# Kernel optimization log

Hardware: AMD Instinct MI355X
Metric: run time of the kernel (lower is better)

## Reference

```python
import jax, jax.numpy as jnp
import numpy as np

N = 4096          # rank / n
OFF_DIAG = 4      # banded half-width
D_IN = 4096       # v: [N, D_IN]
D_OUT = 4096      # u: [D_OUT, N]
BATCH, SEQ = 4, 2048


def _banded_indices(n, off_diag):
    """All (row, col) entries of the 2*off_diag+1 diagonals, like torch.sparse.spdiags."""
    rows, cols = [], []
    for off in range(-off_diag, off_diag + 1):
        if off >= 0:
            i = np.arange(0, n - off)
        else:
            i = np.arange(-off, n)
        rows.append(i)
        cols.append(i + off)
    return np.concatenate(rows).astype(np.int32), np.concatenate(cols).astype(np.int32)


def setup_inputs() -> dict:
    key = jax.random.key(0)
    k_x, k_u, k_v, k_sp, k_s = jax.random.split(key, 5)
    row, col = _banded_indices(N, OFF_DIAG)
    nnz = row.shape[0]  # 36844
    return {
        "x": jax.random.normal(k_x, (BATCH, SEQ, D_IN), dtype=jnp.float32),
        "u": jax.random.normal(k_u, (D_OUT, N), dtype=jnp.float32),
        "v": jax.random.normal(k_v, (N, D_IN), dtype=jnp.float32),
        "s_pre": jax.random.uniform(k_sp, (N,), dtype=jnp.float32),  # singular values (diag)
        # kaiming_normal_ on a [1, nnz] tensor -> std = sqrt(2 / nnz)
        "s": jax.random.normal(k_s, (nnz,), dtype=jnp.float32) * np.float32(np.sqrt(2.0 / nnz)),
        "gate": jnp.zeros((1,), dtype=jnp.float32),
        "row": jnp.asarray(row),
        "col": jnp.asarray(col),
    }


def reference(x, u, v, s_pre, s, gate, row, col):
    n = s_pre.shape[0]
    # del_s = diag(s_pre) + scatter(s * sigmoid(gate)) at banded indices  -> [n, n]
    vals = s * jax.nn.sigmoid(gate)          # [nnz]
    M = jnp.zeros((n, n), dtype=x.dtype).at[row, col].add(vals)
    M = M.at[jnp.arange(n), jnp.arange(n)].add(s_pre)
    # weight = ((del_s @ v).T) @ u.T  -> [D_IN, D_OUT]
    weight = (M @ v).T @ u.T
    return x @ weight
```

## Files before the change

kernel.cpp:

```cpp
#include <hip/hip_runtime.h>
#include <cstdint>

typedef unsigned short u16;
typedef __attribute__((ext_vector_type(8))) __bf16 bf16x8;
typedef __attribute__((ext_vector_type(4))) float f32x4;

#define N_DIM 4096

__device__ __forceinline__ u16 f2bf(float f) {
    union { float f; unsigned u; } c; c.f = f;
    unsigned u = c.u;
    u += 0x7FFFu + ((u >> 16) & 1u);
    return (u16)(u >> 16);
}

__device__ __forceinline__ void gl_lds16(const u16* g, u16* l) {
    __builtin_amdgcn_global_load_lds(
        (const __attribute__((address_space(1))) void*)g,
        (__attribute__((address_space(3))) void*)l, 16, 0, 0);
}

__global__ void band_kernel(const float* __restrict__ s,
                            const float* __restrict__ s_pre,
                            const float* __restrict__ gate,
                            float* __restrict__ bnd) {
    int n = blockIdx.x * blockDim.x + threadIdx.x;
    if (n >= N_DIM) return;
    float sig = 1.0f / (1.0f + __expf(-gate[0]));
    const int base[9] = {0, 4092, 8185, 12279, 16374, 20470, 24565, 28659, 32752};
    #pragma unroll
    for (int o = 0; o < 9; ++o) {
        int off = o - 4;
        int col = n + off;
        float val = 0.0f;
        if (col >= 0 && col < N_DIM) {
            int idx = (off >= 0) ? (base[o] + n) : (base[o] + n + off);
            val = s[idx] * sig;
        }
        if (off == 0) val += s_pre[n];
        bnd[n * 9 + o] = val;
    }
}

__global__ void band_combine_t(const float* __restrict__ v,
                               const float* __restrict__ bnd,
                               u16* __restrict__ P) {
    __shared__ float tile[32][33];
    int n0 = blockIdx.x * 32;
    int d0 = blockIdx.y * 32;
    int tx = threadIdx.x;
    int ty = threadIdx.y;
    #pragma unroll
    for (int i = 0; i < 4; ++i) {
        int nl = ty + 8 * i;
        int n = n0 + nl;
        int d = d0 + tx;
        float acc = 0.0f;
        #pragma unroll
        for (int o = 0; o < 9; ++o) {
            int src = n + o - 4;
            float w = bnd[n * 9 + o];
            float vv = ((unsigned)src < (unsigned)N_DIM) ? v[(size_t)src * N_DIM + d] : 0.0f;
            acc += w * vv;
        }
        tile[nl][tx] = acc;
    }
    __syncthreads();
    #pragma unroll
    for (int i = 0; i < 4; ++i) {
        int dl = ty + 8 * i;
        P[(size_t)(d0 + dl) * N_DIM + (n0 + tx)] = f2bf(tile[tx][dl]);
    }
}

__global__ void cvt_bf16(const float* __restrict__ in, u16* __restrict__ out, int nElem4) {
    int i = blockIdx.x * blockDim.x + threadIdx.x;
    if (i >= nElem4) return;
    float4 f = ((const float4*)in)[i];
    ushort4 o;
    o.x = f2bf(f.x); o.y = f2bf(f.y); o.z = f2bf(f.z); o.w = f2bf(f.w);
    ((ushort4*)out)[i] = o;
}

template <bool OUT_BF16>
__global__ __launch_bounds__(256)
void gemm_tn(const u16* __restrict__ A, const u16* __restrict__ B,
             float* __restrict__ Cf, u16* __restrict__ Cb,
             int M, int N, int K) {
    __shared__ u16 As[128 * 32];
    __shared__ u16 Bs[128 * 32];
    const int tid = threadIdx.x;
    const int lane = tid & 63;
    const int wave = tid >> 6;
    const int wm = wave >> 1;
    const int wn = wave & 1;
    const long m0 = (long)blockIdx.y * 128;
    const long n0 = (long)blockIdx.x * 128;

    const u16* Ab = A + m0 * K;
    const u16* Bb = B + n0 * K;

    f32x4 acc[4][4];
    #pragma unroll
    for (int i = 0; i < 4; ++i)
        #pragma unroll
        for (int j = 0; j < 4; ++j)
            acc[i][j] = (f32x4){0.f, 0.f, 0.f, 0.f};

    const int row = tid >> 2;
    const int kc  = (tid & 3) * 8;

    const int ml = lane & 15;
    const int kq = (lane >> 4) * 8;

    for (int kt = 0; kt < K; kt += 32) {
        __syncthreads();
        gl_lds16(Ab + (long)row * K + kt + kc,        &As[tid * 8]);
        gl_lds16(Ab + (long)(row + 64) * K + kt + kc, &As[2048 + tid * 8]);
        gl_lds16(Bb + (long)row * K + kt + kc,        &Bs[tid * 8]);
        gl_lds16(Bb + (long)(row + 64) * K + kt + kc, &Bs[2048 + tid * 8]);
        __syncthreads();

        bf16x8 af[4], bfr[4];
        #pragma unroll
        for (int i = 0; i < 4; ++i)
            af[i] = *(const bf16x8*)&As[(wm * 64 + i * 16 + ml) * 32 + kq];
        #pragma unroll
        for (int i = 0; i < 4; ++i)
            bfr[i] = *(const bf16x8*)&Bs[(wn * 64 + i * 16 + ml) * 32 + kq];

        #pragma unroll
        for (int mi = 0; mi < 4; ++mi)
            #pragma unroll
            for (int ni = 0; ni < 4; ++ni)
                acc[mi][ni] = __builtin_amdgcn_mfma_f32_16x16x32_bf16(
                    af[mi], bfr[ni], acc[mi][ni], 0, 0, 0);
    }

    const int cn = lane & 15;
    const int rg = lane >> 4;
    #pragma unroll
    for (int mi = 0; mi < 4; ++mi) {
        #pragma unroll
        for (int ni = 0; ni < 4; ++ni) {
            const long mb = m0 + wm * 64 + mi * 16 + rg * 4;
            const long nn = n0 + wn * 64 + ni * 16 + cn;
            #pragma unroll
            for (int r = 0; r < 4; ++r) {
                const long off = (mb + r) * N + nn;
                if (OUT_BF16) Cb[off] = f2bf(acc[mi][ni][r]);
                else          Cf[off] = acc[mi][ni][r];
            }
        }
    }
}

extern "C" void kernel_launch(void* const* d_in, const int* in_sizes, int n_in,
                              void* d_out, int out_size, void* d_ws, size_t ws_size,
                              hipStream_t stream) {
    const float* x     = (const float*)d_in[0];
    const float* u     = (const float*)d_in[1];
    const float* v     = (const float*)d_in[2];
    const float* s_pre = (const float*)d_in[3];
    const float* s     = (const float*)d_in[4];
    const float* gate  = (const float*)d_in[5];
    float* out = (float*)d_out;

    const int BS = 8192;
    const size_t NN = (size_t)N_DIM * N_DIM;

    char* ws = (char*)d_ws;
    float* bnd = (float*)ws;
    u16*   P   = (u16*)(ws + (1 << 18));
    u16*   Ubf = (u16*)(ws + (1 << 18) + NN * 2);
    u16*   Wt  = (u16*)(ws + (1 << 18) + NN * 4);
    u16*   Xbf = (u16*)(ws + (1 << 18) + NN * 6);

    band_kernel<<<16, 256, 0, stream>>>(s, s_pre, gate, bnd);

    band_combine_t<<<dim3(128, 128), dim3(32, 8), 0, stream>>>(v, bnd, P);

    cvt_bf16<<<(int)(NN / 4 / 256), 256, 0, stream>>>(u, Ubf, (int)(NN / 4));
    cvt_bf16<<<(int)((size_t)BS * N_DIM / 4 / 256), 256, 0, stream>>>(
        x, Xbf, (int)((size_t)BS * N_DIM / 4));

    gemm_tn<true><<<dim3(N_DIM / 128, N_DIM / 128), 256, 0, stream>>>(
        Ubf, P, nullptr, Wt, N_DIM, N_DIM, N_DIM);

    gemm_tn<false><<<dim3(N_DIM / 128, BS / 128), 256, 0, stream>>>(
        Xbf, Wt, out, nullptr, BS, N_DIM, N_DIM);
}
```

Baseline: 921.7 us.

## Replace GEMM with 256x256 8-wave double-buffered pipelined MFMA kernel

Replaces the simple 128x128 single-buffered GEMM with a 256x256 tile kernel using 8 waves and double-buffered LDS. Global-to-LDS loads are interleaved with MFMA quadrants under explicit barriers and waitcnts, LDS reads use a swizzled layout to avoid bank conflicts, and workgroups are remapped for L2 locality. The intent is to hide memory latency and raise tensor-core utilization. It costs higher register pressure and 128KB of LDS per block, with hand-tuned sync that could be fragile.

```diff
diff --git a/kernel.cpp b/kernel.cpp
--- a/kernel.cpp
+++ b/kernel.cpp
@@ -82,74 +82,176 @@
     ((ushort4*)out)[i] = o;
 }
 
+#define BARRIER() __builtin_amdgcn_s_barrier()
+#define LGKM0()   asm volatile("s_waitcnt lgkmcnt(0)" ::: "memory")
+#define VMC(n)    asm volatile("s_waitcnt vmcnt(" #n ")" ::: "memory")
+
+#define MFMA_Q(QM, QN) do {                                                   \
+    __builtin_amdgcn_s_setprio(1);                                            \
+    _Pragma("unroll")                                                         \
+    for (int k_ = 0; k_ < 2; ++k_)                                            \
+      _Pragma("unroll")                                                       \
+      for (int i_ = 0; i_ < 4; ++i_)                                          \
+        _Pragma("unroll")                                                     \
+        for (int j_ = 0; j_ < 2; ++j_)                                        \
+          acc[(QM)*4 + i_][(QN)*2 + j_] =                                     \
+            __builtin_amdgcn_mfma_f32_16x16x32_bf16(                          \
+              aR[i_][k_], bR[(QN)*2 + j_][k_],                                \
+              acc[(QM)*4 + i_][(QN)*2 + j_], 0, 0, 0);                        \
+    __builtin_amdgcn_s_setprio(0);                                            \
+  } while (0)
+
 template <bool OUT_BF16>
-__global__ __launch_bounds__(256)
-void gemm_tn(const u16* __restrict__ A, const u16* __restrict__ B,
-             float* __restrict__ Cf, u16* __restrict__ Cb,
-             int M, int N, int K) {
-    __shared__ u16 As[128 * 32];
-    __shared__ u16 Bs[128 * 32];
+__global__ __launch_bounds__(512, 2)
+void gemm_tn8(const u16* __restrict__ A, const u16* __restrict__ B,
+              float* __restrict__ Cf, u16* __restrict__ Cb,
+              int M, int N, int K) {
+    __shared__ __align__(16) u16 As[2][16384];
+    __shared__ __align__(16) u16 Bs[2][16384];
+
     const int tid = threadIdx.x;
-    const int lane = tid & 63;
-    const int wave = tid >> 6;
-    const int wm = wave >> 1;
-    const int wn = wave & 1;
-    const long m0 = (long)blockIdx.y * 128;
-    const long n0 = (long)blockIdx.x * 128;
-
-    const u16* Ab = A + m0 * K;
-    const u16* Bb = B + n0 * K;
-
-    f32x4 acc[4][4];
-    #pragma unroll
-    for (int i = 0; i < 4; ++i)
+    const int l   = tid & 63;
+    const int w   = tid >> 6;
+    const int wm  = w >> 2;
+    const int wn  = w & 3;
+
+    const int nbx = gridDim.x;
+    const int nwg = nbx * gridDim.y;
+    int lid = blockIdx.y * nbx + blockIdx.x;
+    if ((nwg & 7) == 0) lid = (lid & 7) * (nwg >> 3) + (lid >> 3);
+    const long m0 = (long)(lid / nbx) * 256;
+    const long n0 = (long)(lid % nbx) * 256;
+
+    const u16* Ab = A + m0 * (long)K;
+    const u16* Bb = B + n0 * (long)K;
+
+    const int lin16 = (l < 32) ? l : (l ^ 2);
+    const int sr = lin16 >> 2;
+    const int sc = (lin16 & 3) * 8;
+    const int s0 = w;
+    const int s1 = 8 + w;
+    const int g0 = ((s0 >> 1) * 16 + sr) * K + (s0 & 1) * 32 + sc;
+    const int g1 = ((s1 >> 1) * 16 + sr) * K + (s1 & 1) * 32 + sc;
+    const int d0 = s0 * 512 + l * 8;
+    const int d1 = s1 * 512 + l * 8;
+
+    const int foff = (((((l & 15) << 6) + ((l >> 4) << 4)) ^ (((l >> 3) & 1) << 5)) >> 1);
+    const int abase = wm * 8192;
+    const int bbase = wn * 4096;
+
+    f32x4 acc[8][4];
+    #pragma unroll
+    for (int i = 0; i < 8; ++i)
         #pragma unroll
         for (int j = 0; j < 4; ++j)
             acc[i][j] = (f32x4){0.f, 0.f, 0.f, 0.f};
 
-    const int row = tid >> 2;
-    const int kc  = (tid & 3) * 8;
-
-    const int ml = lane & 15;
-    const int kq = (lane >> 4) * 8;
-
-    for (int kt = 0; kt < K; kt += 32) {
-        __syncthreads();
-        gl_lds16(Ab + (long)row * K + kt + kc,        &As[tid * 8]);
-        gl_lds16(Ab + (long)(row + 64) * K + kt + kc, &As[2048 + tid * 8]);
-        gl_lds16(Bb + (long)row * K + kt + kc,        &Bs[tid * 8]);
-        gl_lds16(Bb + (long)(row + 64) * K + kt + kc, &Bs[2048 + tid * 8]);
-        __syncthreads();
-
-        bf16x8 af[4], bfr[4];
+    bf16x8 aR[4][2], bR[4][2];
+
+    auto stageA = [&](int buf, int t, int h) {
+        const u16* g = Ab + (long)h * 128 * K + (long)t * 64;
+        u16* lb = &As[buf][h * 8192];
+        gl_lds16(g + g0, lb + d0);
+        gl_lds16(g + g1, lb + d1);
+    };
+    auto stageB = [&](int buf, int t, int h) {
+        const u16* g = Bb + (long)h * 128 * K + (long)t * 64;
+        u16* lb = &Bs[buf][h * 8192];
+        gl_lds16(g + g0, lb + d0);
+        gl_lds16(g + g1, lb + d1);
+    };
+    auto loadA4 = [&](int buf, int fmBase) {
         #pragma unroll
         for (int i = 0; i < 4; ++i)
-            af[i] = *(const bf16x8*)&As[(wm * 64 + i * 16 + ml) * 32 + kq];
-        #pragma unroll
-        for (int i = 0; i < 4; ++i)
-            bfr[i] = *(const bf16x8*)&Bs[(wn * 64 + i * 16 + ml) * 32 + kq];
-
-        #pragma unroll
-        for (int mi = 0; mi < 4; ++mi)
             #pragma unroll
-            for (int ni = 0; ni < 4; ++ni)
-                acc[mi][ni] = __builtin_amdgcn_mfma_f32_16x16x32_bf16(
-                    af[mi], bfr[ni], acc[mi][ni], 0, 0, 0);
-    }
-
-    const int cn = lane & 15;
-    const int rg = lane >> 4;
-    #pragma unroll
-    for (int mi = 0; mi < 4; ++mi) {
-        #pragma unroll
-        for (int ni = 0; ni < 4; ++ni) {
-            const long mb = m0 + wm * 64 + mi * 16 + rg * 4;
-            const long nn = n0 + wn * 64 + ni * 16 + cn;
+            for (int ks = 0; ks < 2; ++ks)
+                aR[i][ks] = *(const bf16x8*)&As[buf][abase + (fmBase + i) * 1024 + ks * 512 + foff];
+    };
+    auto loadB2 = [&](int buf, int fnBase) {
+        #pragma unroll
+        for (int i = 0; i < 2; ++i)
+            #pragma unroll
+            for (int ks = 0; ks < 2; ++ks)
+                bR[fnBase + i][ks] = *(const bf16x8*)&Bs[buf][bbase + (fnBase + i) * 1024 + ks * 512 + foff];
+    };
+
+    const int NT = K >> 6;
+
+    stageA(0, 0, 0); stageA(0, 0, 1);
+    stageB(0, 0, 0); stageB(0, 0, 1);
+    stageB(1, 1, 0); stageB(1, 1, 1);
+    VMC(4);
+    BARRIER();
+
+    for (int it = 0; it < (NT >> 1); ++it) {
+        const int kt = it * 2;
+        const int t2 = (kt + 2 < NT) ? kt + 2 : NT - 1;
+        const int t3 = (kt + 3 < NT) ? kt + 3 : NT - 1;
+
+        loadA4(0, 0); loadB2(0, 0);
+        stageA(1, kt + 1, 0);
+        BARRIER(); LGKM0();
+        MFMA_Q(0, 0);
+        BARRIER();
+
+        loadB2(0, 2);
+        stageA(1, kt + 1, 1);
+        BARRIER(); LGKM0();
+        MFMA_Q(0, 1);
+        BARRIER();
+
+        loadA4(0, 4);
+        stageB(0, t2, 0);
+        BARRIER(); LGKM0();
+        MFMA_Q(1, 0);
+        BARRIER();
+
+        stageB(0, t2, 1);
+        VMC(4);
+        BARRIER(); LGKM0();
+        MFMA_Q(1, 1);
+        BARRIER();
+
+        loadA4(1, 0); loadB2(1, 0);
+        stageA(0, t2, 0);
+        BARRIER(); LGKM0();
+        MFMA_Q(0, 0);
+        BARRIER();
+
+        loadB2(1, 2);
+        stageA(0, t2, 1);
+        BARRIER(); LGKM0();
+        MFMA_Q(0, 1);
+        BARRIER();
+
+        loadA4(1, 4);
+        stageB(1, t3, 0);
+        BARRIER(); LGKM0();
+        MFMA_Q(1, 0);
+        BARRIER();
+
+        stageB(1, t3, 1);
+        VMC(4);
+        BARRIER(); LGKM0();
+        MFMA_Q(1, 1);
+        BARRIER();
+    }
+
+    VMC(0);
+
+    const int cn = l & 15;
+    const int rg = l >> 4;
+    #pragma unroll
+    for (int fm = 0; fm < 8; ++fm) {
+        #pragma unroll
+        for (int fn = 0; fn < 4; ++fn) {
+            const long mb = m0 + wm * 128 + fm * 16 + rg * 4;
+            const long nn = n0 + wn * 64 + fn * 16 + cn;
             #pragma unroll
             for (int r = 0; r < 4; ++r) {
                 const long off = (mb + r) * N + nn;
-                if (OUT_BF16) Cb[off] = f2bf(acc[mi][ni][r]);
-                else          Cf[off] = acc[mi][ni][r];
+                if (OUT_BF16) Cb[off] = f2bf(acc[fm][fn][r]);
+                else          Cf[off] = acc[fm][fn][r];
             }
         }
     }
@@ -184,9 +286,9 @@
     cvt_bf16<<<(int)((size_t)BS * N_DIM / 4 / 256), 256, 0, stream>>>(
         x, Xbf, (int)((size_t)BS * N_DIM / 4));
 
-    gemm_tn<true><<<dim3(N_DIM / 128, N_DIM / 128), 256, 0, stream>>>(
+    gemm_tn8<true><<<dim3(N_DIM / 256, N_DIM / 256), 512, 0, stream>>>(
         Ubf, P, nullptr, Wt, N_DIM, N_DIM, N_DIM);
 
-    gemm_tn<false><<<dim3(N_DIM / 128, BS / 128), 256, 0, stream>>>(
+    gemm_tn8<false><<<dim3(N_DIM / 256, BS / 256), 512, 0, stream>>>(
         Xbf, Wt, out, nullptr, BS, N_DIM, N_DIM);
 }
```

Measured after the change: 739.9 us. 1.25x faster.
